# Kernel optimization log

Measured on AMD Instinct MI355X. Metric: run time of the kernel, lower is better.

## Reference

```python
import jax, jax.numpy as jnp
import numpy as np

B, C, D, H, W = 4, 1, 192, 192, 192
SMALL = 4            # int(192 * bias_scale=0.025)
BIAS_STD = 0.7
MAX_SIGMA = 3.0
TRUNCATE = 4.0
K = 2 * int(TRUNCATE * MAX_SIGMA) + 1   # fixed truncated kernel size = 25
N_LABELS = 32
TABLE = 128          # static remap-table size (>= max source label, >= max dest)


def setup_inputs() -> dict:
    key = jax.random.key(0)
    k1, k2, k3, k4, k5 = jax.random.split(key, 5)
    return {
        "x": jax.random.normal(k1, (B, C, D, H, W), jnp.float32),
        "small_bias": jax.random.normal(k2, (B, 1, SMALL, SMALL, SMALL), jnp.float32),
        "sigma01": jax.random.uniform(k3, (B, 3), jnp.float32),
        "labels": jax.random.randint(k4, (B, 1, D, H, W), 0, N_LABELS, jnp.int32),
        "source_values": jnp.arange(N_LABELS, dtype=jnp.int64),
        "dest_values": jax.random.randint(k5, (N_LABELS,), 0, 100, jnp.int64),
    }


def _lin_weights(n_in, n_out):
    """Dense 1D linear-interp matrix [n_out, n_in], align_corners=True."""
    pos = jnp.linspace(0.0, n_in - 1.0, n_out)
    i0 = jnp.clip(jnp.floor(pos).astype(jnp.int32), 0, n_in - 2)
    f = pos - i0.astype(pos.dtype)
    r = jnp.arange(n_out)
    Wm = jnp.zeros((n_out, n_in), jnp.float32)
    Wm = Wm.at[r, i0].add(1.0 - f).at[r, i0 + 1].add(f)
    return Wm


def _bias_field(small_bias):
    # trilinear align_corners upsample [B,1,s,s,s] -> [B,1,D,H,W], separable
    b = small_bias * BIAS_STD
    b = jnp.einsum('bcxyz,dx->bcdyz', b, _lin_weights(SMALL, D))
    b = jnp.einsum('bcdyz,hy->bcdhz', b, _lin_weights(SMALL, H))
    b = jnp.einsum('bcdhz,wz->bcdhw', b, _lin_weights(SMALL, W))
    return b


def _gauss_kernels(sigma):
    """sigma [3] -> normalized kernels [3, K]; identity (delta) where sigma<0.01."""
    ar = jnp.arange(K, dtype=jnp.float32) - K // 2
    s = jnp.maximum(sigma, 1e-3)[:, None]
    g = jnp.exp(-0.5 * (ar[None, :] ** 2) / (s ** 2))
    g = g / g.sum(-1, keepdims=True)
    delta = jnp.zeros((K,), jnp.float32).at[K // 2].set(1.0)
    return jnp.where(sigma[:, None] >= 0.01, g, delta[None, :])


def _blur_axis(x, k, axis):
    # x [C,D,H,W]; depthwise 1D conv along `axis` with replicate (edge) padding
    p = K // 2
    xm = jnp.moveaxis(x, axis, -1)
    shp = xm.shape
    xm = xm.reshape(-1, 1, shp[-1])
    xm = jnp.pad(xm, ((0, 0), (0, 0), (p, p)), mode='edge')
    out = jax.lax.conv_general_dilated(xm, k.reshape(1, 1, K), (1,), 'VALID')
    return jnp.moveaxis(out.reshape(shp), -1, axis)


def _blur_sample(x, kernels):
    # x [C,D,H,W], kernels [3,K]; separable blur over D,H,W
    for i, ax in enumerate((1, 2, 3)):
        x = _blur_axis(x, kernels[i], ax)
    return x


def reference(x, small_bias, sigma01, labels, source_values, dest_values):
    # 1) bias-field corruption: x * exp(upsampled random field)
    img = x * jnp.exp(_bias_field(small_bias))
    # 2) dynamic per-sample Gaussian blur, sigma in [0, MAX_SIGMA]
    kernels = jax.vmap(_gauss_kernels)(sigma01 * MAX_SIGMA)   # [B,3,K]
    img = jax.vmap(_blur_sample)(img, kernels)
    # 3) label remap via lookup table gather
    mapping = jnp.zeros((TABLE,), jnp.int32).at[source_values].set(
        dest_values.astype(jnp.int32))
    labels_out = mapping[labels]
    return img, labels_out
```

## Files before the change

kernel.cpp:

```cpp
#include <hip/hip_runtime.h>
#include <hip/hip_fp16.h>
#include <cstdint>
#include <cstddef>

#define Bc 4
#define Dd 192
#define Hh 192
#define Ww 192
#define KK 25
#define RR 12
#define VOL (Bc*Dd*Hh*Ww)
#define SP 216
#define SPU (SP/2)
#define SH 98
#define RIN 56
#define RD  56

typedef unsigned short u16;
typedef unsigned int   u32;
typedef __fp16 h2 __attribute__((ext_vector_type(2)));
typedef __fp16 h8 __attribute__((ext_vector_type(8)));
typedef float  f32x4 __attribute__((ext_vector_type(4)));

__device__ inline u32 pk2(float a, float b) {
    return __builtin_bit_cast(u32, __builtin_amdgcn_cvt_pkrtz(a, b));
}

__device__ inline float gauss_tap(float s01, int idx) {
    float sig = s01 * 3.0f;
    float s = fmaxf(sig, 1e-3f);
    float inv2 = -0.5f / (s * s);
    float sum = 0.0f;
    #pragma unroll
    for (int i = 0; i < KK; i++) {
        float a = (float)(i - RR);
        sum += __expf(a * a * inv2);
    }
    float a = (float)(idx - RR);
    float v = __expf(a * a * inv2) / sum;
    if (sig < 0.01f) v = (idx == RR) ? 1.0f : 0.0f;
    return v;
}

__global__ __launch_bounds__(256) void pass_wh_remap_kernel(
    const float* __restrict__ x, u16* __restrict__ outB,
    const float* __restrict__ sigma01, const float* __restrict__ sb,
    const int* __restrict__ src, const int* __restrict__ dst,
    const int4* __restrict__ labels, float4* __restrict__ lab_out) {
    __shared__ u16 P[RIN * SP];
    __shared__ float2 ch2[RIN * 3];
    __shared__ u16 kpadW[64];
    __shared__ u32 khp[25];
    __shared__ float Lmap[128];
    const int tid = threadIdx.x;
    const int hx = blockIdx.x;
    const int d  = blockIdx.y;
    const int b  = blockIdx.z;

    if (tid < RIN) {
        int r = tid;
        int hrow = min(max(32 * hx - RR + r, 0), Hh - 1);
        float pos_d = d * (3.0f / 191.0f);
        int   id0   = min((int)pos_d, 2);
        float fd    = pos_d - (float)id0;
        float pos_h = hrow * (3.0f / 191.0f);
        int   ih0   = min((int)pos_h, 2);
        float fh    = pos_h - (float)ih0;
        const float* sbA = sb + b * 64 + id0 * 16 + ih0 * 4;
        float c[4];
        #pragma unroll
        for (int k = 0; k < 4; k++) {
            float v00 = sbA[k],      v01 = sbA[4 + k];
            float v10 = sbA[16 + k], v11 = sbA[20 + k];
            float vd0 = (1.f - fd) * v00 + fd * v10;
            float vd1 = (1.f - fd) * v01 + fd * v11;
            c[k] = ((1.f - fh) * vd0 + fh * vd1) * 0.7f;
        }
        #pragma unroll
        for (int k = 0; k < 3; k++)
            ch2[r * 3 + k] = make_float2(c[k], c[k + 1] - c[k]);
    }
    if (tid >= 56 && tid < 184) Lmap[tid - 56] = 0.0f;
    if (tid >= 56 && tid < 81) {
        int i = tid - 56;
        float v = gauss_tap(sigma01[b * 3 + 1], i);
        u16 hb = __builtin_bit_cast(u16, __float2half(v));
        khp[i] = (u32)hb | ((u32)hb << 16);
    }
    if (tid >= 184 && tid < 248) {
        int i = tid - 184;
        int tt = i - 15;
        u16 v = 0;
        if (tt >= 0 && tt < KK)
            v = __builtin_bit_cast(u16, __float2half(gauss_tap(sigma01[b * 3 + 2], tt)));
        kpadW[i] = v;
    }
    __syncthreads();

    if (tid < 32) {
        int s = src[tid];
        if (s >= 0 && s < 128) Lmap[s] = (float)dst[tid];
    }

    const size_t pbase = ((size_t)b * Dd + d) * (size_t)(Hh * Ww);
    {
        const int w4 = tid % 48;
        const int rloc = tid / 48;
        const int w = 4 * w4;
        float fwj[4];
        int   selj[4];
        #pragma unroll
        for (int j = 0; j < 4; j++) {
            float pw = (float)(w + j) * (3.0f / 191.0f);
            int sel = (pw >= 1.0f) + (pw >= 2.0f);
            selj[j] = sel;
            fwj[j] = pw - (float)sel;
        }
        #pragma unroll
        for (int it = 0; it < 12; it++) {
            int row = it * 5 + rloc;
            if (tid < 240 && row < RIN) {
                int hrow = min(max(32 * hx - RR + row, 0), Hh - 1);
                float4 v = *(const float4*)(x + pbase + (size_t)hrow * Ww + w);
                float rs[4];
                #pragma unroll
                for (int j = 0; j < 4; j++) {
                    float2 cd = ch2[row * 3 + selj[j]];
                    float bias = fmaf(fwj[j], cd.y, cd.x);
                    float val = (j == 0 ? v.x : j == 1 ? v.y : j == 2 ? v.z : v.w);
                    rs[j] = val * __expf(bias);
                }
                u32* dstp = (u32*)&P[row * SP + RR + w];
                dstp[0] = pk2(rs[0], rs[1]);
                dstp[1] = pk2(rs[2], rs[3]);
                if (w4 == 0) {
                    u32 hh = pk2(rs[0], rs[0]);
                    u32* hp = (u32*)&P[row * SP];
                    #pragma unroll
                    for (int m = 0; m < 6; m++) hp[m] = hh;
                } else if (w4 == 47) {
                    u32 hh = pk2(rs[3], rs[3]);
                    u32* hp = (u32*)&P[row * SP + RR + Ww];
                    #pragma unroll
                    for (int m = 0; m < 6; m++) hp[m] = hh;
                }
            }
        }
    }
    __syncthreads();

    {
        const int bid = (b * Dd + d) * 6 + hx;
        const int4* lp = labels + (size_t)bid * 1536 + tid;
        int4 lab[6];
        #pragma unroll
        for (int m = 0; m < 6; m++) lab[m] = lp[m * 256];
        float4* op = lab_out + (size_t)bid * 1536 + tid;
        #pragma unroll
        for (int m = 0; m < 6; m++) {
            int4 l = lab[m];
            float4 o;
            o.x = Lmap[min(max(l.x, 0), 127)];
            o.y = Lmap[min(max(l.y, 0), 127)];
            o.z = Lmap[min(max(l.z, 0), 127)];
            o.w = Lmap[min(max(l.w, 0), 127)];
            op[m * 256] = o;
        }
    }

    {
        const int ln = tid & 63, wv = tid >> 6;
        const int c  = ln & 15;
        const int kg = ln >> 4;
        h8 B0, B1;
        #pragma unroll
        for (int j = 0; j < 8; j++) {
            int k = kg * 8 + j;
            B0[j] = __builtin_bit_cast(__fp16, kpadW[15 + k - c]);
            int i1 = 15 + k + 32 - c;
            B1[j] = __builtin_bit_cast(__fp16, (i1 < 64) ? kpadW[i1] : (u16)0);
        }
        const int ra = min(wv * 16 + c, RIN - 1);
        const u16* rowp = &P[ra * SP + kg * 8];
        const int rd0 = wv * 16 + kg * 4;
        h8 F[10];
        #pragma unroll
        for (int f = 0; f < 10; f++)
            F[f] = __builtin_bit_cast(h8, *(const uint4*)(rowp + f * 16));
        #pragma unroll
        for (int ct = 0; ct < 8; ct++) {
            f32x4 acc = {0.f, 0.f, 0.f, 0.f};
            acc = __builtin_amdgcn_mfma_f32_16x16x32_f16(F[ct], B0, acc, 0, 0, 0);
            acc = __builtin_amdgcn_mfma_f32_16x16x32_f16(F[ct + 2], B1, acc, 0, 0, 0);
            #pragma unroll
            for (int m = 0; m < 4; m++) {
                int rd = rd0 + m;
                if (rd < RIN)
                    P[rd * SP + RR + ct * 16 + c] =
                        __builtin_bit_cast(u16, (__fp16)acc[m]);
            }
        }
        h8 G[4];
        G[0] = __builtin_bit_cast(h8, *(const uint4*)(rowp + 160));
        G[1] = __builtin_bit_cast(h8, *(const uint4*)(rowp + 176));
        G[2] = __builtin_bit_cast(h8, *(const uint4*)(rowp + ((kg == 0) ? 192 : 160)));
        G[3] = __builtin_bit_cast(h8, *(const uint4*)(rowp + ((kg == 0) ? 208 : 160)));
        #pragma unroll
        for (int ct = 8; ct < 12; ct++) {
            h8 A0 = (ct < 10) ? F[ct] : G[ct - 10];
            h8 A1 = G[ct - 8];
            f32x4 acc = {0.f, 0.f, 0.f, 0.f};
            acc = __builtin_amdgcn_mfma_f32_16x16x32_f16(A0, B0, acc, 0, 0, 0);
            acc = __builtin_amdgcn_mfma_f32_16x16x32_f16(A1, B1, acc, 0, 0, 0);
            #pragma unroll
            for (int m = 0; m < 4; m++) {
                int rd = rd0 + m;
                if (rd < RIN)
                    P[rd * SP + RR + ct * 16 + c] =
                        __builtin_bit_cast(u16, (__fp16)acc[m]);
            }
        }
    }
    __syncthreads();

    {
        u32 khr[KK];
        #pragma unroll
        for (int t = 0; t < KK; t++) khr[t] = khp[t];
        u32* outp = (u32*)(outB + pbase);
        #pragma unroll
        for (int it = 0; it < 2; it++) {
            int item = it * 256 + tid;
            if (item < 384) {
                int col = item % 96;
                int g = item / 96;
                u32 win[32];
                #pragma unroll
                for (int i = 0; i < 32; i++)
                    win[i] = *((const u32*)P + (g * 8 + i) * SPU + 6 + col);
                h2 acc[8];
                #pragma unroll
                for (int j = 0; j < 8; j++) acc[j] = (h2)(0.0f);
                #pragma unroll
                for (int t = 0; t < KK; t++) {
                    h2 kv = __builtin_bit_cast(h2, khr[t]);
                    #pragma unroll
                    for (int j = 0; j < 8; j++)
                        acc[j] += kv * __builtin_bit_cast(h2, win[j + t]);
                }
                #pragma unroll
                for (int j = 0; j < 8; j++)
                    outp[(32 * hx + g * 8 + j) * 96 + col] =
                        __builtin_bit_cast(u32, acc[j]);
            }
        }
    }
}

__global__ __launch_bounds__(192) void pass_d_kernel(
    const u16* __restrict__ in, float* __restrict__ img,
    const float* __restrict__ sigma01) {
    __shared__ __attribute__((aligned(16))) u16 T[RD * SH];
    __shared__ u32 kdp[25];
    const int tid = threadIdx.x;
    const int w0 = blockIdx.x * 96;
    const int d0 = blockIdx.y * 32;
    const int z = blockIdx.z;
    const int h = z % Hh, b = z / Hh;
    if (tid < 25) {
        float v = gauss_tap(sigma01[b * 3 + 0], tid);
        u16 hb = __builtin_bit_cast(u16, __float2half(v));
        kdp[tid] = (u32)hb | ((u32)hb << 16);
    }
    #pragma unroll
    for (int k = 0; k < 4; k++) {
        int idx = k * 192 + tid;
        if (idx < RD * 12) {
            int r = idx / 12, sg = idx % 12;
            int dd = min(max(d0 + r - RR, 0), Dd - 1);
            uint4 v = *(const uint4*)(in + (((size_t)b * Dd + dd) * Hh + h) * (size_t)Ww + w0 + sg * 8);
            u32* p = (u32*)&T[r * SH + sg * 8];
            p[0] = v.x; p[1] = v.y; p[2] = v.z; p[3] = v.w;
        }
    }
    __syncthreads();
    u32 kdr[KK];
    #pragma unroll
    for (int t = 0; t < KK; t++) kdr[t] = kdp[t];
    const int p = tid % 48;
    const int g = tid / 48;
    const int ob = g * 8;
    u32 win[32];
    #pragma unroll
    for (int i = 0; i < 32; i++) win[i] = *(const u32*)&T[(ob + i) * SH + 2 * p];
    h2 acc[8];
    #pragma unroll
    for (int j = 0; j < 8; j++) acc[j] = (h2)(0.0f);
    #pragma unroll
    for (int t = 0; t < KK; t++) {
        h2 kv = __builtin_bit_cast(h2, kdr[t]);
        #pragma unroll
        for (int j = 0; j < 8; j++)
            acc[j] += kv * __builtin_bit_cast(h2, win[j + t]);
    }
    #pragma unroll
    for (int j = 0; j < 8; j++) {
        h2 a = acc[j];
        float2 f = make_float2((float)a.x, (float)a.y);
        *(float2*)(img + (((size_t)b * Dd + (d0 + ob + j)) * Hh + h) * (size_t)Ww + w0 + 2 * p) = f;
    }
}

extern "C" void kernel_launch(void* const* d_in, const int* in_sizes, int n_in,
                              void* d_out, int out_size, void* d_ws, size_t ws_size,
                              hipStream_t stream) {
    const float* x          = (const float*)d_in[0];
    const float* small_bias = (const float*)d_in[1];
    const float* sigma01    = (const float*)d_in[2];
    const int*   labels     = (const int*)d_in[3];
    const int*   src        = (const int*)d_in[4];
    const int*   dst        = (const int*)d_in[5];

    float* out     = (float*)d_out;
    float* img     = out;
    float* lab_out = out + (size_t)VOL;
    u16*   Bb      = (u16*)((char*)d_ws + 8192);

    pass_wh_remap_kernel<<<dim3(6, Dd, Bc), 256, 0, stream>>>(
        x, Bb, sigma01, small_bias, src, dst,
        (const int4*)labels, (float4*)lab_out);
    pass_d_kernel<<<dim3(Ww / 96, Dd / 32, Bc * Hh), 192, 0, stream>>>(
        Bb, img, sigma01);
}
```

Before: 128.3 us.

## Double W/H tile height to 64 rows and specialize waves for label remap

The fused W/H-blur kernel now processes 64 output rows per block with 512 threads instead of 32 rows with 256. The 12-row halo on each side is amortized over more rows, which cuts redundant x loads, bias exps and MFMA work per output. The label remap is moved onto two dedicated waves so it runs alongside the six MFMA waves instead of before them. The bias coefficients are now stored as a float4 per row with select logic, in place of precomputed float2 pairs. The grid has half as many blocks with higher LDS and register use per block, which may lower occupancy.

```diff
diff --git a/kernel.cpp b/kernel.cpp
--- a/kernel.cpp
+++ b/kernel.cpp
@@ -13,7 +13,7 @@
 #define SP 216
 #define SPU (SP/2)
 #define SH 98
-#define RIN 56
+#define RIN 88
 #define RD  56
 
 typedef unsigned short u16;
@@ -42,13 +42,13 @@
     return v;
 }
 
-__global__ __launch_bounds__(256) void pass_wh_remap_kernel(
+__global__ __launch_bounds__(512) void pass_wh_remap_kernel(
     const float* __restrict__ x, u16* __restrict__ outB,
     const float* __restrict__ sigma01, const float* __restrict__ sb,
     const int* __restrict__ src, const int* __restrict__ dst,
     const int4* __restrict__ labels, float4* __restrict__ lab_out) {
-    __shared__ u16 P[RIN * SP];
-    __shared__ float2 ch2[RIN * 3];
+    __shared__ __attribute__((aligned(16))) u16 P[RIN * SP];
+    __shared__ __attribute__((aligned(16))) float ch[RIN][4];
     __shared__ u16 kpadW[64];
     __shared__ u32 khp[25];
     __shared__ float Lmap[128];
@@ -59,7 +59,7 @@
 
     if (tid < RIN) {
         int r = tid;
-        int hrow = min(max(32 * hx - RR + r, 0), Hh - 1);
+        int hrow = min(max(64 * hx - RR + r, 0), Hh - 1);
         float pos_d = d * (3.0f / 191.0f);
         int   id0   = min((int)pos_d, 2);
         float fd    = pos_d - (float)id0;
@@ -67,28 +67,24 @@
         int   ih0   = min((int)pos_h, 2);
         float fh    = pos_h - (float)ih0;
         const float* sbA = sb + b * 64 + id0 * 16 + ih0 * 4;
-        float c[4];
         #pragma unroll
         for (int k = 0; k < 4; k++) {
             float v00 = sbA[k],      v01 = sbA[4 + k];
             float v10 = sbA[16 + k], v11 = sbA[20 + k];
             float vd0 = (1.f - fd) * v00 + fd * v10;
             float vd1 = (1.f - fd) * v01 + fd * v11;
-            c[k] = ((1.f - fh) * vd0 + fh * vd1) * 0.7f;
-        }
-        #pragma unroll
-        for (int k = 0; k < 3; k++)
-            ch2[r * 3 + k] = make_float2(c[k], c[k + 1] - c[k]);
-    }
-    if (tid >= 56 && tid < 184) Lmap[tid - 56] = 0.0f;
-    if (tid >= 56 && tid < 81) {
-        int i = tid - 56;
+            ch[r][k] = ((1.f - fh) * vd0 + fh * vd1) * 0.7f;
+        }
+    }
+    if (tid >= 96 && tid < 224) Lmap[tid - 96] = 0.0f;
+    if (tid >= 224 && tid < 249) {
+        int i = tid - 224;
         float v = gauss_tap(sigma01[b * 3 + 1], i);
         u16 hb = __builtin_bit_cast(u16, __float2half(v));
         khp[i] = (u32)hb | ((u32)hb << 16);
     }
-    if (tid >= 184 && tid < 248) {
-        int i = tid - 184;
+    if (tid >= 256 && tid < 320) {
+        int i = tid - 256;
         int tt = i - 15;
         u16 v = 0;
         if (tt >= 0 && tt < KK)
@@ -108,25 +104,28 @@
         const int rloc = tid / 48;
         const int w = 4 * w4;
         float fwj[4];
-        int   selj[4];
+        bool  s1j[4], s2j[4];
         #pragma unroll
         for (int j = 0; j < 4; j++) {
             float pw = (float)(w + j) * (3.0f / 191.0f);
-            int sel = (pw >= 1.0f) + (pw >= 2.0f);
-            selj[j] = sel;
-            fwj[j] = pw - (float)sel;
-        }
-        #pragma unroll
-        for (int it = 0; it < 12; it++) {
-            int row = it * 5 + rloc;
-            if (tid < 240 && row < RIN) {
-                int hrow = min(max(32 * hx - RR + row, 0), Hh - 1);
+            bool s1 = pw >= 1.0f, s2 = pw >= 2.0f;
+            s1j[j] = s1; s2j[j] = s2;
+            float fb = s2 ? 2.0f : (s1 ? 1.0f : 0.0f);
+            fwj[j] = pw - fb;
+        }
+        #pragma unroll
+        for (int it = 0; it < 9; it++) {
+            int row = it * 10 + rloc;
+            if (rloc < 10 && row < RIN) {
+                int hrow = min(max(64 * hx - RR + row, 0), Hh - 1);
                 float4 v = *(const float4*)(x + pbase + (size_t)hrow * Ww + w);
+                float4 cv = *(const float4*)&ch[row][0];
                 float rs[4];
                 #pragma unroll
                 for (int j = 0; j < 4; j++) {
-                    float2 cd = ch2[row * 3 + selj[j]];
-                    float bias = fmaf(fwj[j], cd.y, cd.x);
+                    float clo = s2j[j] ? cv.z : (s1j[j] ? cv.y : cv.x);
+                    float chi = s2j[j] ? cv.w : (s1j[j] ? cv.z : cv.y);
+                    float bias = fmaf(fwj[j], chi - clo, clo);
                     float val = (j == 0 ? v.x : j == 1 ? v.y : j == 2 ? v.z : v.w);
                     rs[j] = val * __expf(bias);
                 }
@@ -150,74 +149,79 @@
     __syncthreads();
 
     {
-        const int bid = (b * Dd + d) * 6 + hx;
-        const int4* lp = labels + (size_t)bid * 1536 + tid;
-        int4 lab[6];
-        #pragma unroll
-        for (int m = 0; m < 6; m++) lab[m] = lp[m * 256];
-        float4* op = lab_out + (size_t)bid * 1536 + tid;
-        #pragma unroll
-        for (int m = 0; m < 6; m++) {
-            int4 l = lab[m];
-            float4 o;
-            o.x = Lmap[min(max(l.x, 0), 127)];
-            o.y = Lmap[min(max(l.y, 0), 127)];
-            o.z = Lmap[min(max(l.z, 0), 127)];
-            o.w = Lmap[min(max(l.w, 0), 127)];
-            op[m * 256] = o;
-        }
-    }
-
-    {
-        const int ln = tid & 63, wv = tid >> 6;
-        const int c  = ln & 15;
-        const int kg = ln >> 4;
-        h8 B0, B1;
-        #pragma unroll
-        for (int j = 0; j < 8; j++) {
-            int k = kg * 8 + j;
-            B0[j] = __builtin_bit_cast(__fp16, kpadW[15 + k - c]);
-            int i1 = 15 + k + 32 - c;
-            B1[j] = __builtin_bit_cast(__fp16, (i1 < 64) ? kpadW[i1] : (u16)0);
-        }
-        const int ra = min(wv * 16 + c, RIN - 1);
-        const u16* rowp = &P[ra * SP + kg * 8];
-        const int rd0 = wv * 16 + kg * 4;
-        h8 F[10];
-        #pragma unroll
-        for (int f = 0; f < 10; f++)
-            F[f] = __builtin_bit_cast(h8, *(const uint4*)(rowp + f * 16));
-        #pragma unroll
-        for (int ct = 0; ct < 8; ct++) {
-            f32x4 acc = {0.f, 0.f, 0.f, 0.f};
-            acc = __builtin_amdgcn_mfma_f32_16x16x32_f16(F[ct], B0, acc, 0, 0, 0);
-            acc = __builtin_amdgcn_mfma_f32_16x16x32_f16(F[ct + 2], B1, acc, 0, 0, 0);
-            #pragma unroll
-            for (int m = 0; m < 4; m++) {
-                int rd = rd0 + m;
-                if (rd < RIN)
-                    P[rd * SP + RR + ct * 16 + c] =
-                        __builtin_bit_cast(u16, (__fp16)acc[m]);
-            }
-        }
-        h8 G[4];
-        G[0] = __builtin_bit_cast(h8, *(const uint4*)(rowp + 160));
-        G[1] = __builtin_bit_cast(h8, *(const uint4*)(rowp + 176));
-        G[2] = __builtin_bit_cast(h8, *(const uint4*)(rowp + ((kg == 0) ? 192 : 160)));
-        G[3] = __builtin_bit_cast(h8, *(const uint4*)(rowp + ((kg == 0) ? 208 : 160)));
-        #pragma unroll
-        for (int ct = 8; ct < 12; ct++) {
-            h8 A0 = (ct < 10) ? F[ct] : G[ct - 10];
-            h8 A1 = G[ct - 8];
-            f32x4 acc = {0.f, 0.f, 0.f, 0.f};
-            acc = __builtin_amdgcn_mfma_f32_16x16x32_f16(A0, B0, acc, 0, 0, 0);
-            acc = __builtin_amdgcn_mfma_f32_16x16x32_f16(A1, B1, acc, 0, 0, 0);
-            #pragma unroll
-            for (int m = 0; m < 4; m++) {
-                int rd = rd0 + m;
-                if (rd < RIN)
-                    P[rd * SP + RR + ct * 16 + c] =
-                        __builtin_bit_cast(u16, (__fp16)acc[m]);
+        const int wv = tid >> 6;
+        if (wv < 6) {
+            const int ln = tid & 63;
+            const int c  = ln & 15;
+            const int kg = ln >> 4;
+            h8 B0, B1;
+            #pragma unroll
+            for (int j = 0; j < 8; j++) {
+                int k = kg * 8 + j;
+                B0[j] = __builtin_bit_cast(__fp16, kpadW[15 + k - c]);
+                int i1 = 15 + k + 32 - c;
+                B1[j] = __builtin_bit_cast(__fp16, (i1 < 64) ? kpadW[i1] : (u16)0);
+            }
+            const int ra = min(wv * 16 + c, RIN - 1);
+            const u16* rowp = &P[ra * SP + kg * 8];
+            const int rd0 = wv * 16 + kg * 4;
+            h8 F[10];
+            #pragma unroll
+            for (int f = 0; f < 10; f++)
+                F[f] = __builtin_bit_cast(h8, *(const uint4*)(rowp + f * 16));
+            #pragma unroll
+            for (int ct = 0; ct < 8; ct++) {
+                f32x4 acc = {0.f, 0.f, 0.f, 0.f};
+                acc = __builtin_amdgcn_mfma_f32_16x16x32_f16(F[ct], B0, acc, 0, 0, 0);
+                acc = __builtin_amdgcn_mfma_f32_16x16x32_f16(F[ct + 2], B1, acc, 0, 0, 0);
+                #pragma unroll
+                for (int m = 0; m < 4; m++) {
+                    int rd = rd0 + m;
+                    if (rd < RIN)
+                        P[rd * SP + RR + ct * 16 + c] =
+                            __builtin_bit_cast(u16, (__fp16)acc[m]);
+                }
+            }
+            h8 G[4];
+            G[0] = __builtin_bit_cast(h8, *(const uint4*)(rowp + 160));
+            G[1] = __builtin_bit_cast(h8, *(const uint4*)(rowp + 176));
+            G[2] = __builtin_bit_cast(h8, *(const uint4*)(rowp + ((kg == 0) ? 192 : 160)));
+            G[3] = __builtin_bit_cast(h8, *(const uint4*)(rowp + ((kg == 0) ? 208 : 160)));
+            #pragma unroll
+            for (int ct = 8; ct < 12; ct++) {
+                h8 A0 = (ct < 10) ? F[ct] : G[ct - 10];
+                h8 A1 = G[ct - 8];
+                f32x4 acc = {0.f, 0.f, 0.f, 0.f};
+                acc = __builtin_amdgcn_mfma_f32_16x16x32_f16(A0, B0, acc, 0, 0, 0);
+                acc = __builtin_amdgcn_mfma_f32_16x16x32_f16(A1, B1, acc, 0, 0, 0);
+                #pragma unroll
+                for (int m = 0; m < 4; m++) {
+                    int rd = rd0 + m;
+                    if (rd < RIN)
+                        P[rd * SP + RR + ct * 16 + c] =
+                            __builtin_bit_cast(u16, (__fp16)acc[m]);
+                }
+            }
+        } else {
+            const int idx = tid - 384;
+            const int bid = (b * Dd + d) * 3 + hx;
+            const size_t base = (size_t)bid * 3072 + idx;
+            #pragma unroll
+            for (int chk = 0; chk < 4; chk++) {
+                int4 lab[6];
+                #pragma unroll
+                for (int m = 0; m < 6; m++)
+                    lab[m] = labels[base + (size_t)(chk * 6 + m) * 128];
+                #pragma unroll
+                for (int m = 0; m < 6; m++) {
+                    int4 l = lab[m];
+                    float4 o;
+                    o.x = Lmap[min(max(l.x, 0), 127)];
+                    o.y = Lmap[min(max(l.y, 0), 127)];
+                    o.z = Lmap[min(max(l.z, 0), 127)];
+                    o.w = Lmap[min(max(l.w, 0), 127)];
+                    lab_out[base + (size_t)(chk * 6 + m) * 128] = o;
+                }
             }
         }
     }
@@ -230,8 +234,8 @@
         u32* outp = (u32*)(outB + pbase);
         #pragma unroll
         for (int it = 0; it < 2; it++) {
-            int item = it * 256 + tid;
-            if (item < 384) {
+            int item = it * 512 + tid;
+            if (item < 768) {
                 int col = item % 96;
                 int g = item / 96;
                 u32 win[32];
@@ -250,7 +254,7 @@
                 }
                 #pragma unroll
                 for (int j = 0; j < 8; j++)
-                    outp[(32 * hx + g * 8 + j) * 96 + col] =
+                    outp[(64 * hx + g * 8 + j) * 96 + col] =
                         __builtin_bit_cast(u32, acc[j]);
             }
         }
@@ -326,7 +330,7 @@
     float* lab_out = out + (size_t)VOL;
     u16*   Bb      = (u16*)((char*)d_ws + 8192);
 
-    pass_wh_remap_kernel<<<dim3(6, Dd, Bc), 256, 0, stream>>>(
+    pass_wh_remap_kernel<<<dim3(3, Dd, Bc), 512, 0, stream>>>(
         x, Bb, sigma01, small_bias, src, dst,
         (const int4*)labels, (float4*)lab_out);
     pass_d_kernel<<<dim3(Ww / 96, Dd / 32, Bc * Hh), 192, 0, stream>>>(
```

Measured after the change: 130.5 us. Within noise of the previous version (+1.7%).
